# Performance work log

Hardware: AMD Instinct MI355X
Metric: run time of the kernel (lower is better)

Reference implementation:

```python
import jax, jax.numpy as jnp
import numpy as np

L = 4      # number of Verifier layers in the linked list
D = 1536   # constraint matrix dimension


def setup_inputs() -> dict:
    key = jax.random.key(0)
    ks = jax.random.split(key, 6)
    scale = 0.02  # keep chained matmul magnitudes sane
    lb = jax.random.normal(ks[0], (1, D), jnp.float32)
    ub = lb + jax.random.uniform(ks[1], (1, D), jnp.float32)  # ensure lb <= ub
    lcs = scale * jax.random.normal(ks[2], (L, D, D), jnp.float32)
    ucs = lcs + scale * jax.random.uniform(ks[3], (L, D, D), jnp.float32)
    lc_bias = jax.random.normal(ks[4], (L, D), jnp.float32)
    uc_bias = lc_bias + jax.random.uniform(ks[5], (L, D), jnp.float32)
    return {"lb": lb, "ub": ub, "lcs": lcs, "ucs": ucs,
            "lc_bias": lc_bias, "uc_bias": uc_bias}


def reference(lb, ub, lcs, ucs, lc_bias, uc_bias):
    pos = lambda x: jnp.maximum(x, 0.0)
    neg = lambda x: jnp.minimum(x, 0.0)
    n_layers = lcs.shape[0]

    # Layer 0 forward: its backsubstitution returns these bounds unchanged
    # (prev is None), and all later backsubs terminate on these stored bounds.
    lb0 = lb @ pos(lcs[0]).T + ub @ neg(lcs[0]).T + lc_bias[0]
    ub0 = ub @ pos(ucs[0]).T + lb @ neg(ucs[0]).T + uc_bias[0]
    cur_lb, cur_ub = lb0, ub0

    for k in range(1, n_layers):
        # backsubstitution from layer k: start with transposed constraint
        C_lc, C_uc = lcs[k].T, ucs[k].T           # [D, D]
        C_lcb, C_ucb = lc_bias[k], uc_bias[k]     # [D]
        # recurse through layers k-1 .. 0, combining constraints
        for j in range(k - 1, -1, -1):
            pU, nU = pos(C_uc), neg(C_uc)
            pL, nL = pos(C_lc), neg(C_lc)
            new_ucb = uc_bias[j] @ pU + lc_bias[j] @ nU + C_ucb
            new_uc = ucs[j].T @ pU + lcs[j].T @ nU
            new_lcb = lc_bias[j] @ pL + uc_bias[j] @ nL + C_lcb
            new_lc = lcs[j].T @ pL + ucs[j].T @ nL
            C_lc, C_uc, C_lcb, C_ucb = new_lc, new_uc, new_lcb, new_ucb
        # apply combined constraint to layer-0 stored bounds
        cur_lb = lb0 @ pos(C_lc) + ub0 @ neg(C_lc) + C_lcb
        cur_ub = ub0 @ pos(C_uc) + lb0 @ neg(C_uc) + C_ucb

    return cur_lb, cur_ub
```

## Files before the change

### kernel.cpp

```cpp
#include <hip/hip_runtime.h>

#define D 1536
#define BT 96
#define BK 64
#define NT (D / BK)
#define TT 64
#define TILE_E (BT * BK)
#define BUF_E (3 * TILE_E)

typedef unsigned short u16;
typedef short bf16x8 __attribute__((ext_vector_type(8)));
typedef float f32x4 __attribute__((ext_vector_type(4)));

static __device__ __forceinline__ u16 f2bf(float f) {
    unsigned u; __builtin_memcpy(&u, &f, 4);
    unsigned r = (u + 0x7FFFu + ((u >> 16) & 1u)) >> 16;
    return (u16)r;
}
static __device__ __forceinline__ float bf2f(u16 s) {
    unsigned u = ((unsigned)s) << 16;
    float f; __builtin_memcpy(&f, &u, 4); return f;
}

#define GLDS(g, s) __builtin_amdgcn_global_load_lds( \
    (const __attribute__((address_space(1))) void*)(g), \
    (__attribute__((address_space(3))) void*)(s), 16, 0, 0)

#define MFMA16(a, b, c) __builtin_amdgcn_mfma_f32_16x16x32_bf16(a, b, c, 0, 0, 0)

__global__ __launch_bounds__(256) void prep_k(
    const float* __restrict__ lcs, const float* __restrict__ ucs,
    u16* __restrict__ BsT, u16* __restrict__ BdT,
    u16* __restrict__ Ga, u16* __restrict__ Gc)
{
    const int z = blockIdx.z;
    const int r0 = blockIdx.y * TT, c0 = blockIdx.x * TT;
    const int tid = threadIdx.x;

    if (z == 3) {
#pragma unroll
        for (int m = 0; m < 2; ++m) {
            const float* src = (m ? lcs : ucs) + (size_t)3 * D * D;
            u16* dst = m ? Gc : Ga;
#pragma unroll
            for (int i = 0; i < 2; ++i) {
                int r = (tid >> 3) + i * 32, cc = (tid & 7) * 8;
                const float* p = src + (size_t)(r0 + r) * D + c0 + cc;
                f32x4 x0 = *(const f32x4*)p;
                f32x4 x1 = *(const f32x4*)(p + 4);
                bf16x8 y;
#pragma unroll
                for (int e = 0; e < 4; ++e) { y[e] = (short)f2bf(x0[e]); y[e + 4] = (short)f2bf(x1[e]); }
                *(bf16x8*)(dst + (size_t)(r0 + r) * D + c0 + cc) = y;
            }
        }
        return;
    }

    __shared__ u16 ts[TT][TT + 8];
    __shared__ u16 td[TT][TT + 8];
    const float* srcl = lcs + (size_t)z * D * D;
    const float* srcu = ucs + (size_t)z * D * D;
#pragma unroll
    for (int i = 0; i < 2; ++i) {
        int c = tid + i * 256; int r = c >> 3, v = c & 7;
        size_t off = (size_t)(r0 + r) * D + c0 + v * 8;
        f32x4 l0 = *(const f32x4*)(srcl + off);
        f32x4 l1 = *(const f32x4*)(srcl + off + 4);
        f32x4 u0 = *(const f32x4*)(srcu + off);
        f32x4 u1 = *(const f32x4*)(srcu + off + 4);
        bf16x8 ys, yd;
#pragma unroll
        for (int e = 0; e < 4; ++e) {
            ys[e]     = (short)f2bf((u0[e] + l0[e]) * 0.5f);
            yd[e]     = (short)f2bf((u0[e] - l0[e]) * 0.5f);
            ys[e + 4] = (short)f2bf((u1[e] + l1[e]) * 0.5f);
            yd[e + 4] = (short)f2bf((u1[e] - l1[e]) * 0.5f);
        }
        *(bf16x8*)&ts[r][v * 8] = ys;
        *(bf16x8*)&td[r][v * 8] = yd;
    }
    __syncthreads();
#pragma unroll
    for (int i = 0; i < 2; ++i) {
        int c = tid + i * 256; int rr = c >> 3, v = c & 7;
        bf16x8 xs, xd;
#pragma unroll
        for (int e = 0; e < 8; ++e) { xs[e] = (short)ts[v * 8 + e][rr]; xd[e] = (short)td[v * 8 + e][rr]; }
        size_t off = (size_t)z * D * D + (size_t)(c0 + rr) * D + r0 + v * 8;
        *(bf16x8*)(BsT + off) = xs;
        *(bf16x8*)(BdT + off) = xd;
    }
}

__global__ __launch_bounds__(256) void vec_k(
    const float* __restrict__ lb, const float* __restrict__ ub,
    const float* __restrict__ lcs, const float* __restrict__ ucs,
    const float* __restrict__ lcb, const float* __restrict__ ucb,
    float* __restrict__ lb0, float* __restrict__ ub0,
    float* __restrict__ cb_uc, float* __restrict__ cb_lc)
{
    const int tt = blockIdx.x * 4 + (threadIdx.x >> 6);
    const int lane = threadIdx.x & 63;
    const int which = tt / D;
    const int row_n = tt - which * D;

    const float* row; const float* vp; const float* vn;
    if (which == 0)      { row = lcs + (size_t)row_n * D;               vp = lb;           vn = ub; }
    else if (which == 1) { row = ucs + (size_t)row_n * D;               vp = ub;           vn = lb; }
    else if (which == 2) { row = ucs + (size_t)(3 * (size_t)D * D) + (size_t)row_n * D; vp = ucb + 2 * D; vn = lcb + 2 * D; }
    else                 { row = lcs + (size_t)(3 * (size_t)D * D) + (size_t)row_n * D; vp = lcb + 2 * D; vn = ucb + 2 * D; }

    float s = 0.f;
    for (int c2 = 0; c2 < D / 256; ++c2) {
        int base = (c2 * 64 + lane) * 4;
        f32x4 g = *(const f32x4*)(row + base);
        f32x4 p = *(const f32x4*)(vp + base);
        f32x4 m = *(const f32x4*)(vn + base);
#pragma unroll
        for (int e = 0; e < 4; ++e) s += g[e] * (g[e] > 0.f ? p[e] : m[e]);
    }
#pragma unroll
    for (int o = 32; o; o >>= 1) s += __shfl_down(s, o);
    if (lane == 0) {
        if (which == 0)      lb0[row_n] = s + lcb[row_n];
        else if (which == 1) ub0[row_n] = s + ucb[row_n];
        else if (which == 2) cb_uc[row_n] = s + ucb[3 * D + row_n];
        else                 cb_lc[row_n] = s + lcb[3 * D + row_n];
    }
}

__global__ __launch_bounds__(256, 2) void gemm_step(
    const u16* __restrict__ Guc, const u16* __restrict__ Glc,
    const u16* __restrict__ Bs, const u16* __restrict__ Bd,
    u16* __restrict__ outU, u16* __restrict__ outL,
    const float* __restrict__ ucbN, const float* __restrict__ lcbN,
    float* __restrict__ cb_uc, float* __restrict__ cb_lc)
{
    __shared__ u16 smem[2 * BUF_E];
    const int wg  = blockIdx.x + 16 * blockIdx.y + 256 * blockIdx.z;
    const int xcd = wg & 7, idx = wg >> 3;
    const int chain = xcd >> 2;
    const int bx = (xcd & 1) * 8 + (idx & 7);
    const int by = ((xcd >> 1) & 1) * 8 + (idx >> 3);

    const u16* A = chain ? Glc : Guc;
    u16* out = chain ? outL : outU;
    const unsigned sgn = chain ? 0x80008000u : 0u;
    const int r0 = by * BT, c0 = bx * BT;
    const int tid = threadIdx.x, lane = tid & 63, wid = tid >> 6;
    const int mb = (wid >> 1) * 48, nb = (wid & 1) * 48;
    const int lrow = lane & 15, lk = lane >> 4;

    f32x4 acc[3][3] = {};

#define STAGE(kt, sbuf) do { \
    _Pragma("unroll") for (int i_ = 0; i_ < 9; ++i_) { \
        const int idx_ = (i_ % 3) * 256 + tid; \
        const int row_ = idx_ >> 3; \
        const int kcg_ = (tid & 7) ^ (row_ & 7); \
        const u16* base_ = (i_ < 3) ? (A + (size_t)(r0 + row_) * D) \
                        : ((i_ < 6) ? (Bs + (size_t)(c0 + row_) * D) \
                                    : (Bd + (size_t)(c0 + row_) * D)); \
        GLDS(base_ + (kt) + kcg_ * 8, (char*)(sbuf) + (i_ * 256 + wid * 64) * 16); \
    } } while (0)

    STAGE(0, smem);
    STAGE(BK, smem + BUF_E);

#pragma unroll 1
    for (int t = 0; t < NT; ++t) {
        if (t < NT - 1) { asm volatile("s_waitcnt vmcnt(9)" ::: "memory"); }
        else            { asm volatile("s_waitcnt vmcnt(0)" ::: "memory"); }
        __builtin_amdgcn_sched_barrier(0);
        __builtin_amdgcn_s_barrier();

        const u16* sb = smem + (t & 1) * BUF_E;
#pragma unroll
        for (int ks = 0; ks < 2; ++ks) {
            const int slot = ks * 4;
            bf16x8 a[3], x[3];
#pragma unroll
            for (int mi = 0; mi < 3; ++mi) {
                int row = mb + mi * 16 + lrow;
                a[mi] = *(const bf16x8*)(sb + row * BK + ((slot + lk) ^ (row & 7)) * 8);
                union { bf16x8 v; unsigned u[4]; } ti, to;
                ti.v = a[mi];
#pragma unroll
                for (int q = 0; q < 4; ++q) to.u[q] = (ti.u[q] & 0x7FFF7FFFu) ^ sgn;
                x[mi] = to.v;
            }
#pragma unroll
            for (int ni = 0; ni < 3; ++ni) {
                int row = nb + ni * 16 + lrow;
                int o = row * BK + ((slot + lk) ^ (row & 7)) * 8;
                bf16x8 bs = *(const bf16x8*)(sb + TILE_E + o);
                bf16x8 bd = *(const bf16x8*)(sb + 2 * TILE_E + o);
#pragma unroll
                for (int mi = 0; mi < 3; ++mi) {
                    acc[mi][ni] = MFMA16(a[mi], bs, acc[mi][ni]);
                    acc[mi][ni] = MFMA16(x[mi], bd, acc[mi][ni]);
                }
            }
        }
        __builtin_amdgcn_s_barrier();
        if (t + 2 < NT)
            STAGE((t + 2) * BK, smem + (t & 1) * BUF_E);
    }

    if (ucbN) {
        const float* pb_ = chain ? lcbN : ucbN;
        const float* nb_ = chain ? ucbN : lcbN;
        float* cb = chain ? cb_lc : cb_uc;
        float pbv[3], nbv[3];
#pragma unroll
        for (int ni = 0; ni < 3; ++ni) {
            int c = c0 + nb + ni * 16 + lrow;
            pbv[ni] = pb_[c]; nbv[ni] = nb_[c];
        }
#pragma unroll
        for (int mi = 0; mi < 3; ++mi)
#pragma unroll
            for (int q = 0; q < 4; ++q) {
                float s = 0.f;
#pragma unroll
                for (int ni = 0; ni < 3; ++ni) {
                    float g = acc[mi][ni][q];
                    s += g * (g > 0.f ? pbv[ni] : nbv[ni]);
                }
                s += __shfl_xor(s, 1); s += __shfl_xor(s, 2);
                s += __shfl_xor(s, 4); s += __shfl_xor(s, 8);
                if (lrow == 0)
                    atomicAdd(&cb[r0 + mb + mi * 16 + lk * 4 + q], s);
            }
    }

#pragma unroll
    for (int mi = 0; mi < 3; ++mi)
#pragma unroll
        for (int ni = 0; ni < 3; ++ni) {
            int c = c0 + nb + ni * 16 + lrow;
            int rbase = r0 + mb + mi * 16 + lk * 4;
#pragma unroll
            for (int q = 0; q < 4; ++q)
                out[(size_t)(rbase + q) * D + c] = f2bf(acc[mi][ni][q]);
        }
#undef STAGE
}

__global__ __launch_bounds__(256) void final_k(
    const u16* __restrict__ Guc, const u16* __restrict__ Glc,
    const float* __restrict__ cb_uc, const float* __restrict__ cb_lc,
    const float* __restrict__ lb0, const float* __restrict__ ub0,
    float* __restrict__ out)
{
    const int gw = blockIdx.x * 4 + (threadIdx.x >> 6);
    const int lane = threadIdx.x & 63;
    const int which = gw >= D;
    const int n = which ? gw - D : gw;
    const u16* row = (which ? Guc : Glc) + (size_t)n * D;
    const float* vp = which ? ub0 : lb0;
    const float* vn = which ? lb0 : ub0;
    float s = 0.f;
    for (int c2 = 0; c2 < D / 512; ++c2) {
        int base = (c2 * 64 + lane) * 8;
        bf16x8 g8 = *(const bf16x8*)(row + base);
        f32x4 p0 = *(const f32x4*)(vp + base);
        f32x4 p1 = *(const f32x4*)(vp + base + 4);
        f32x4 n0 = *(const f32x4*)(vn + base);
        f32x4 n1 = *(const f32x4*)(vn + base + 4);
#pragma unroll
        for (int e = 0; e < 8; ++e) {
            float g = bf2f((u16)g8[e]);
            float pv = e < 4 ? p0[e] : p1[e - 4];
            float nv = e < 4 ? n0[e] : n1[e - 4];
            s += g * (g > 0.f ? pv : nv);
        }
    }
#pragma unroll
    for (int o = 32; o; o >>= 1) s += __shfl_down(s, o);
    if (lane == 0) {
        float b = (which ? cb_uc : cb_lc)[n];
        out[which * D + n] = s + b;
    }
}

extern "C" void kernel_launch(void* const* d_in, const int* in_sizes, int n_in,
                              void* d_out, int out_size, void* d_ws, size_t ws_size,
                              hipStream_t stream) {
    const float* lb  = (const float*)d_in[0];
    const float* ub  = (const float*)d_in[1];
    const float* lcs = (const float*)d_in[2];
    const float* ucs = (const float*)d_in[3];
    const float* lcb = (const float*)d_in[4];
    const float* ucb = (const float*)d_in[5];
    float* out = (float*)d_out;

    const size_t DD = (size_t)D * D;
    u16* ws   = (u16*)d_ws;
    u16* BsT = ws;
    u16* BdT = BsT + 3 * DD;
    u16* Ga = BdT + 3 * DD;
    u16* Gb = Ga + DD;
    u16* Gc = Gb + DD;
    u16* Gd = Gc + DD;
    float* fbuf  = (float*)(Gd + DD);
    float* lb0   = fbuf;
    float* ub0   = fbuf + D;
    float* cb_uc = fbuf + 2 * D;
    float* cb_lc = fbuf + 3 * D;

    prep_k<<<dim3(D / TT, D / TT, 4), 256, 0, stream>>>(lcs, ucs, BsT, BdT, Ga, Gc);
    vec_k<<<dim3(4 * D / 4), 256, 0, stream>>>(lb, ub, lcs, ucs, lcb, ucb, lb0, ub0, cb_uc, cb_lc);

    u16* curU = Ga; u16* curL = Gc;
    u16* altU = Gb; u16* altL = Gd;
    for (int j = 2; j >= 0; --j) {
        const float* ucbN = (j > 0) ? (ucb + (size_t)(j - 1) * D) : nullptr;
        const float* lcbN = (j > 0) ? (lcb + (size_t)(j - 1) * D) : nullptr;
        gemm_step<<<dim3(16, 16, 2), 256, 0, stream>>>(
            curU, curL, BsT + (size_t)j * DD, BdT + (size_t)j * DD, altU, altL,
            ucbN, lcbN, cb_uc, cb_lc);
        u16* t;
        t = curU; curU = altU; altU = t;
        t = curL; curL = altL; altL = t;
    }
    final_k<<<dim3(2 * D / 4), 256, 0, stream>>>(curU, curL, cb_uc, cb_lc, lb0, ub0, out);
}
```

Measured before the change: 129.7 us.

## Fuse final bound application into last GEMM epilogue and skip its matrix store

```diff
diff --git a/kernel.cpp b/kernel.cpp
--- a/kernel.cpp
+++ b/kernel.cpp
@@ -208,7 +208,7 @@
             STAGE((t + 2) * BK, smem + (t & 1) * BUF_E);
     }
 
-    if (ucbN) {
+    {
         const float* pb_ = chain ? lcbN : ucbN;
         const float* nb_ = chain ? ucbN : lcbN;
         float* cb = chain ? cb_lc : cb_uc;
@@ -235,54 +235,28 @@
             }
     }
 
-#pragma unroll
-    for (int mi = 0; mi < 3; ++mi)
-#pragma unroll
-        for (int ni = 0; ni < 3; ++ni) {
-            int c = c0 + nb + ni * 16 + lrow;
-            int rbase = r0 + mb + mi * 16 + lk * 4;
-#pragma unroll
-            for (int q = 0; q < 4; ++q)
-                out[(size_t)(rbase + q) * D + c] = f2bf(acc[mi][ni][q]);
-        }
+    if (out) {
+#pragma unroll
+        for (int mi = 0; mi < 3; ++mi)
+#pragma unroll
+            for (int ni = 0; ni < 3; ++ni) {
+                int c = c0 + nb + ni * 16 + lrow;
+                int rbase = r0 + mb + mi * 16 + lk * 4;
+#pragma unroll
+                for (int q = 0; q < 4; ++q)
+                    out[(size_t)(rbase + q) * D + c] = f2bf(acc[mi][ni][q]);
+            }
+    }
 #undef STAGE
 }
 
-__global__ __launch_bounds__(256) void final_k(
-    const u16* __restrict__ Guc, const u16* __restrict__ Glc,
+__global__ __launch_bounds__(256) void emit_k(
     const float* __restrict__ cb_uc, const float* __restrict__ cb_lc,
-    const float* __restrict__ lb0, const float* __restrict__ ub0,
     float* __restrict__ out)
 {
-    const int gw = blockIdx.x * 4 + (threadIdx.x >> 6);
-    const int lane = threadIdx.x & 63;
-    const int which = gw >= D;
-    const int n = which ? gw - D : gw;
-    const u16* row = (which ? Guc : Glc) + (size_t)n * D;
-    const float* vp = which ? ub0 : lb0;
-    const float* vn = which ? lb0 : ub0;
-    float s = 0.f;
-    for (int c2 = 0; c2 < D / 512; ++c2) {
-        int base = (c2 * 64 + lane) * 8;
-        bf16x8 g8 = *(const bf16x8*)(row + base);
-        f32x4 p0 = *(const f32x4*)(vp + base);
-        f32x4 p1 = *(const f32x4*)(vp + base + 4);
-        f32x4 n0 = *(const f32x4*)(vn + base);
-        f32x4 n1 = *(const f32x4*)(vn + base + 4);
-#pragma unroll
-        for (int e = 0; e < 8; ++e) {
-            float g = bf2f((u16)g8[e]);
-            float pv = e < 4 ? p0[e] : p1[e - 4];
-            float nv = e < 4 ? n0[e] : n1[e - 4];
-            s += g * (g > 0.f ? pv : nv);
-        }
-    }
-#pragma unroll
-    for (int o = 32; o; o >>= 1) s += __shfl_down(s, o);
-    if (lane == 0) {
-        float b = (which ? cb_uc : cb_lc)[n];
-        out[which * D + n] = s + b;
-    }
+    int i = blockIdx.x * 256 + threadIdx.x;
+    if (i < D)          out[i] = cb_lc[i];
+    else if (i < 2 * D) out[i] = cb_uc[i - D];
 }
 
 extern "C" void kernel_launch(void* const* d_in, const int* in_sizes, int n_in,
@@ -316,14 +290,16 @@
     u16* curU = Ga; u16* curL = Gc;
     u16* altU = Gb; u16* altL = Gd;
     for (int j = 2; j >= 0; --j) {
-        const float* ucbN = (j > 0) ? (ucb + (size_t)(j - 1) * D) : nullptr;
-        const float* lcbN = (j > 0) ? (lcb + (size_t)(j - 1) * D) : nullptr;
+        const float* ucbN = (j > 0) ? (ucb + (size_t)(j - 1) * D) : ub0;
+        const float* lcbN = (j > 0) ? (lcb + (size_t)(j - 1) * D) : lb0;
+        u16* oU = (j > 0) ? altU : (u16*)nullptr;
+        u16* oL = (j > 0) ? altL : (u16*)nullptr;
         gemm_step<<<dim3(16, 16, 2), 256, 0, stream>>>(
-            curU, curL, BsT + (size_t)j * DD, BdT + (size_t)j * DD, altU, altL,
+            curU, curL, BsT + (size_t)j * DD, BdT + (size_t)j * DD, oU, oL,
             ucbN, lcbN, cb_uc, cb_lc);
         u16* t;
         t = curU; curU = altU; altU = t;
         t = curL; curL = altL; altL = t;
     }
-    final_k<<<dim3(2 * D / 4), 256, 0, stream>>>(curU, curL, cb_uc, cb_lc, lb0, ub0, out);
-}
+    emit_k<<<dim3((2 * D + 255) / 256), 256, 0, stream>>>(cb_uc, cb_lc, out);
+}
```

Measured after the change: 129.9 us. Within noise of the previous version (+0.1%).
